# Optimization experiments

Measured on AMD Instinct MI355X. Metric: run time of the kernel, lower is better.

Reference implementation:

```python
import jax, jax.numpy as jnp
import numpy as np
import itertools

B = 262144  # batch of 16-d vectors to quantize

_BW = np.array([
    [4,0,0,0,0,0,0,0,0,0,0,0,0,0,0,0],[2,2,0,0,0,0,0,0,0,0,0,0,0,0,0,0],
    [2,0,2,0,0,0,0,0,0,0,0,0,0,0,0,0],[2,0,0,2,0,0,0,0,0,0,0,0,0,0,0,0],
    [2,0,0,0,2,0,0,0,0,0,0,0,0,0,0,0],[2,0,0,0,0,2,0,0,0,0,0,0,0,0,0,0],
    [2,0,0,0,0,0,2,0,0,0,0,0,0,0,0,0],[2,0,0,0,0,0,0,2,0,0,0,0,0,0,0,0],
    [2,0,0,0,0,0,0,0,2,0,0,0,0,0,0,0],[2,0,0,0,0,0,0,0,0,2,0,0,0,0,0,0],
    [2,0,0,0,0,0,0,0,0,0,2,0,0,0,0,0],[1,1,1,1,0,1,0,1,1,0,0,1,0,0,0,0],
    [0,1,1,1,1,0,1,0,1,1,0,0,1,0,0,0],[0,0,1,1,1,1,0,1,0,1,1,0,0,1,0,0],
    [0,0,0,1,1,1,1,0,1,0,1,1,0,0,1,0],[1,1,1,1,1,1,1,1,1,1,1,1,1,1,1,1]], dtype=np.float64)

_RM14_G = np.array([
    [1,1,1,1,0,1,0,1,1,0,0,1,0,0,0,0],
    [0,1,1,1,1,0,1,0,1,1,0,0,1,0,0,0],
    [0,0,1,1,1,1,0,1,0,1,1,0,0,1,0,0],
    [0,0,0,1,1,1,1,0,1,0,1,1,0,0,1,0],
    [1,1,1,1,1,1,1,1,1,1,1,1,1,1,1,1]], dtype=np.float64)


def _make_a_and_codebook():
    G = _BW
    vol = np.sqrt(np.linalg.det(G @ G.T))
    a = float(1.0 / vol ** (1.0 / 16.0))
    bits = np.array(list(itertools.product([0, 1], repeat=5)), dtype=np.float64)  # (32,5)
    C = bits @ _RM14_G  # (32,16)
    return a, C


def setup_inputs() -> dict:
    key = jax.random.key(0)
    a, C = _make_a_and_codebook()
    x_in = jax.random.normal(key, (B, 16), dtype=jnp.float32)
    return {
        "x_in": x_in,
        "C_rep": jnp.asarray(C, dtype=jnp.float32),
        "a": jnp.asarray([a], dtype=jnp.float32),
    }


def _d2_quantize(x_in):
    # Closest point in 2*D16: round x/2, fix parity by re-rounding the worst coord.
    x = x_in * 0.5                                   # (N,16)
    f = jnp.round(x)                                 # round-half-to-even, matches torch
    parity = jnp.mod(jnp.sum(f, axis=1), 2.0) == 1.0 # (N,)
    col = jnp.argmax(jnp.abs(x - f), axis=1)         # (N,) first max, matches torch
    onehot = col[:, None] == jnp.arange(x.shape[1])  # (N,16)
    xc = jnp.sum(jnp.where(onehot, x, 0.0), axis=1)  # x at worst coord
    fc = jnp.sum(jnp.where(onehot, f, 0.0), axis=1)  # f at worst coord
    corr = jnp.ceil(xc) + jnp.floor(xc) - fc         # flip rounding direction
    f = jnp.where(onehot & parity[:, None], corr[:, None], f)
    return 2.0 * f


def reference(x_in, C_rep, a):
    x = x_in / a                                     # (B,16)
    diffs = x[:, None, :] - C_rep[None, :, :]        # (B,32,16)
    fq = _d2_quantize(diffs.reshape(-1, 16)).reshape(-1, 32, 16)
    X = fq + C_rep[None, :, :]                       # (B,32,16) candidate points
    D = jnp.sum((X - x[:, None, :]) ** 2, axis=2)    # (B,32) squared distances
    idx = jnp.argmin(D, axis=1)                      # (B,)
    y = jnp.take_along_axis(X, idx[:, None, None], axis=1)[:, 0, :]
    return y * a
```

## Files before the change

kernel.cpp:

```cpp
#include <hip/hip_runtime.h>


constexpr int G5[5][16] = {
    {1,1,1,1,0,1,0,1,1,0,0,1,0,0,0,0},
    {0,1,1,1,1,0,1,0,1,1,0,0,1,0,0,0},
    {0,0,1,1,1,1,0,1,0,1,1,0,0,1,0,0},
    {0,0,0,1,1,1,1,0,1,0,1,1,0,0,1,0},
    {1,1,1,1,1,1,1,1,1,1,1,1,1,1,1,1}};

struct Tabs {
  int m[16];
  unsigned w[32];
  int pt[16];
};
constexpr Tabs make_tabs() {
  Tabs t{};
  for (int j = 0; j < 16; ++j) {
    int m = 0;
    for (int i = 0; i < 5; ++i) m |= G5[i][j] << (4 - i);
    t.m[j] = m;
    t.pt[j] = (G5[0][j] << 3) | (G5[1][j] << 2) | (G5[2][j] << 1) | G5[3][j];
  }
  for (int k = 0; k < 32; ++k) {
    unsigned om = 0, p2 = 0;
    for (int j = 0; j < 16; ++j) {
      int c = 0;
      for (int i = 0; i < 5; ++i) c += ((k >> (4 - i)) & 1) * G5[i][j];
      om |= (unsigned)(c & 1) << j;
      p2 ^= (unsigned)((c >> 1) & 1);
    }
    t.w[k] = om | (p2 << 16);
  }
  return t;
}
constexpr Tabs tb = make_tabs();

__device__ __forceinline__ int parity16i(const float (&f)[16]) {
  float s0 = ((f[0] + f[1]) + (f[2] + f[3])) + ((f[4] + f[5]) + (f[6] + f[7]));
  float s1 = ((f[8] + f[9]) + (f[10] + f[11])) + ((f[12] + f[13]) + (f[14] + f[15]));
  return ((int)(s0 + s1)) & 1;
}

template <bool EMIT>
__device__ __forceinline__ float eval_k(int kk, const float (&xh)[16], float a,
                                        float (&y)[16], const float (*Cs)[16]) {
#pragma clang fp contract(off)
  float cf[16];
  {
    const float4* crow = reinterpret_cast<const float4*>(&Cs[kk][0]);
    float4 c0 = crow[0], c1 = crow[1], c2 = crow[2], c3 = crow[3];
    cf[0] = c0.x; cf[1] = c0.y; cf[2] = c0.z; cf[3] = c0.w;
    cf[4] = c1.x; cf[5] = c1.y; cf[6] = c1.z; cf[7] = c1.w;
    cf[8] = c2.x; cf[9] = c2.y; cf[10] = c2.z; cf[11] = c2.w;
    cf[12] = c3.x; cf[13] = c3.y; cf[14] = c3.z; cf[15] = c3.w;
  }
  float f[16], dd[16];
#pragma unroll
  for (int j = 0; j < 16; ++j) {
    float x2 = __builtin_fmaf(cf[j], -0.5f, xh[j]);
    float fj = __builtin_rintf(x2);
    f[j] = fj;
    dd[j] = x2 - fj;
  }
  const int par = parity16i(f);

  float tv[16];
  int ti[16];
#pragma unroll
  for (int j = 0; j < 16; ++j) { tv[j] = __builtin_fabsf(dd[j]); ti[j] = 1 << j; }
#pragma unroll
  for (int w = 8; w >= 1; w >>= 1) {
#pragma unroll
    for (int j = 0; j < w; ++j) {
      bool L = tv[2 * j] >= tv[2 * j + 1];
      tv[j] = L ? tv[2 * j] : tv[2 * j + 1];
      ti[j] = L ? ti[2 * j] : ti[2 * j + 1];
    }
  }
  const int ohm = par ? ti[0] : 0;

  float sq[16];
#pragma unroll
  for (int j = 0; j < 16; ++j) {
    float X  = __builtin_fmaf(2.0f, f[j], cf[j]);
    float s2 = __builtin_copysignf(2.0f, dd[j]);
    float bitf = (float)((ohm >> j) & 1);
    float Xp = __builtin_fmaf(bitf, s2, X);
    float e  = __builtin_fmaf(-2.0f, xh[j], Xp);
    sq[j] = e * e;
    if (EMIT) y[j] = Xp * a;
  }
  float r0 = sq[0] + sq[8],  r1 = sq[1] + sq[9];
  float r2 = sq[2] + sq[10], r3 = sq[3] + sq[11];
  float r4 = sq[4] + sq[12], r5 = sq[5] + sq[13];
  float r6 = sq[6] + sq[14], r7 = sq[7] + sq[15];
  return ((r0 + r1) + (r2 + r3)) + ((r4 + r5) + (r6 + r7));
}

__global__ __launch_bounds__(256, 4) void bw_quant_kernel(
    const float* __restrict__ x_in,
    const float* __restrict__ C_rep,
    const float* __restrict__ a_ptr,
    float* __restrict__ y_out,
    int n_rows)
{
#pragma clang fp contract(off)
  __shared__ alignas(16) float Cs[32][16];
  for (int i = threadIdx.x; i < 32 * 16; i += 256)
    Cs[i >> 4][i & 15] = (float)__builtin_popcount((i >> 4) & tb.m[i & 15]);
  __syncthreads();

  const int row = blockIdx.x * 256 + threadIdx.x;
  if (row >= n_rows) return;

  const float a = a_ptr[0];

  float dd0[16], dd1[16], g[16], sq0[16];
  int P0 = 0, P1 = 0;
  {
    const float4* xr4 = reinterpret_cast<const float4*>(x_in + (size_t)row * 16);
    float xv[16];
#pragma unroll
    for (int q = 0; q < 4; ++q) {
      float4 v = xr4[q];
      xv[q * 4 + 0] = v.x; xv[q * 4 + 1] = v.y;
      xv[q * 4 + 2] = v.z; xv[q * 4 + 3] = v.w;
    }
#pragma unroll
    for (int j = 0; j < 16; ++j) {
      float xj = xv[j] / a;
      float xh = xj * 0.5f;
      float t0 = __builtin_rintf(xh);
      dd0[j] = xh - t0;
      float hm = xh - 0.5f;
      float t1 = __builtin_rintf(hm);
      dd1[j] = hm - t1;
      P0 |= ((int)t0 & 1) << j;
      P1 |= ((int)t1 & 1) << j;
      sq0[j] = dd0[j] * dd0[j];
      g[tb.pt[j]] = __builtin_fmaf(dd1[j], dd1[j], -sq0[j]);
    }
  }
  float S0 = (((sq0[0] + sq0[1]) + (sq0[2] + sq0[3])) + ((sq0[4] + sq0[5]) + (sq0[6] + sq0[7])))
           + (((sq0[8] + sq0[9]) + (sq0[10] + sq0[11])) + ((sq0[12] + sq0[13]) + (sq0[14] + sq0[15])));

#pragma unroll
  for (int s = 1; s < 16; s <<= 1) {
#pragma unroll
    for (int p = 0; p < 16; ++p) {
      if (!(p & s)) {
        float u = g[p], v = g[p | s];
        g[p] = u + v;
        g[p | s] = u - v;
      }
    }
  }
  float S1 = S0 + g[0];
  float h[16];
  h[0] = 0.0f;
#pragma unroll
  for (int t = 1; t < 16; ++t) h[t] = 0.5f * (g[0] - g[t]);

  float b1 = __builtin_inff(), b2 = b1, b3 = b1;
  int k1 = 0, k2 = 0, k3 = 0;

#pragma unroll
  for (int k = 0; k < 32; ++k) {
    const unsigned w = tb.w[k];
    const unsigned O = w & 0xFFFFu;
    const int p2 = (int)(w >> 16);
    const int kap = k >> 1;

    float s = (k & 1) ? (S1 - h[kap]) : (S0 + h[kap]);

    float d[16];
#pragma unroll
    for (int j = 0; j < 16; ++j)
      d[j] = ((O >> j) & 1u) ? dd1[j] : dd0[j];

    float t0 = __builtin_fmaxf(__builtin_fmaxf(__builtin_fabsf(d[0]),  __builtin_fabsf(d[1])),  __builtin_fabsf(d[2]));
    float t1 = __builtin_fmaxf(__builtin_fmaxf(__builtin_fabsf(d[3]),  __builtin_fabsf(d[4])),  __builtin_fabsf(d[5]));
    float t2 = __builtin_fmaxf(__builtin_fmaxf(__builtin_fabsf(d[6]),  __builtin_fabsf(d[7])),  __builtin_fabsf(d[8]));
    float t3 = __builtin_fmaxf(__builtin_fmaxf(__builtin_fabsf(d[9]),  __builtin_fabsf(d[10])), __builtin_fabsf(d[11]));
    float t4 = __builtin_fmaxf(__builtin_fmaxf(__builtin_fabsf(d[12]), __builtin_fabsf(d[13])), __builtin_fabsf(d[14]));
    float mx = __builtin_fmaxf(__builtin_fmaxf(__builtin_fmaxf(t0, t1), t2),
                               __builtin_fmaxf(__builtin_fmaxf(t3, t4), __builtin_fabsf(d[15])));

    unsigned sel = (O & (unsigned)P1) | (~O & (unsigned)P0);
    int cnt = __builtin_popcount(sel) + p2;
    float spen = s + __builtin_fmaf(-2.0f, mx, 1.0f);
    float dtil = (cnt & 1) ? spen : s;

    bool lt1 = dtil < b1, lt2 = dtil < b2, lt3 = dtil < b3;
    float nb3 = lt3 ? (lt2 ? b2 : dtil) : b3;  int nk3 = lt3 ? (lt2 ? k2 : k) : k3;
    float nb2 = lt2 ? (lt1 ? b1 : dtil) : b2;  int nk2 = lt2 ? (lt1 ? k1 : k) : k2;
    b3 = nb3; k3 = nk3;
    b2 = nb2; k2 = nk2;
    b1 = lt1 ? dtil : b1;  k1 = lt1 ? k : k1;
  }

  float xh[16];
  {
    const float4* xr4 = reinterpret_cast<const float4*>(x_in + (size_t)row * 16);
#pragma unroll
    for (int q = 0; q < 4; ++q) {
      float4 v = xr4[q];
      xh[q * 4 + 0] = (v.x / a) * 0.5f;
      xh[q * 4 + 1] = (v.y / a) * 0.5f;
      xh[q * 4 + 2] = (v.z / a) * 0.5f;
      xh[q * 4 + 3] = (v.w / a) * 0.5f;
    }
  }

  float ydummy[16];
  float D1 = eval_k<false>(k1, xh, a, ydummy, Cs);
  float D2 = eval_k<false>(k2, xh, a, ydummy, Cs);
  float D3 = eval_k<false>(k3, xh, a, ydummy, Cs);

  bool c2 = (D2 < D1) || (D2 == D1 && k2 < k1);
  float Db = c2 ? D2 : D1;
  int kb = c2 ? k2 : k1;
  bool c3 = (D3 < Db) || (D3 == Db && k3 < kb);
  kb = c3 ? k3 : kb;

  float y[16];
  (void)eval_k<true>(kb, xh, a, y, Cs);

  float4* yr4 = reinterpret_cast<float4*>(y_out + (size_t)row * 16);
#pragma unroll
  for (int q = 0; q < 4; ++q) {
    float4 v;
    v.x = y[q * 4 + 0]; v.y = y[q * 4 + 1];
    v.z = y[q * 4 + 2]; v.w = y[q * 4 + 3];
    yr4[q] = v;
  }
}

extern "C" void kernel_launch(void* const* d_in, const int* in_sizes, int n_in,
                              void* d_out, int out_size, void* d_ws, size_t ws_size,
                              hipStream_t stream) {
  const float* x_in  = (const float*)d_in[0];
  const float* C_rep = (const float*)d_in[1];
  const float* a_ptr = (const float*)d_in[2];
  float* y_out = (float*)d_out;

  const int n_rows = in_sizes[0] / 16;
  const int block = 256;
  const int grid = (n_rows + block - 1) / block;
  bw_quant_kernel<<<grid, block, 0, stream>>>(x_in, C_rep, a_ptr, y_out, n_rows);
}
```

Before: 24.33 us.

## Compute per-coset max and parity via butterfly transforms; drop the re-evaluation pass

Replaces the per-candidate 16-element select and max tree in the 32-coset loop with a Hadamard-style max butterfly over permuted |d0|/|d1| arrays, which yields the max for all 16 coset pairs at once. Parity per candidate is precomputed into a 32-bit mask from row-mask popcounts. The rescored top-3 candidates now emit their outputs directly instead of running a fourth evaluation. x/2 is staged in shared memory rather than reloaded and divided again. This adds 17 KB of LDS per block, which may limit occupancy, and keeps more live registers for the output candidates.

```diff
diff --git a/kernel.cpp b/kernel.cpp
--- a/kernel.cpp
+++ b/kernel.cpp
@@ -10,8 +10,9 @@
 
 struct Tabs {
   int m[16];
-  unsigned w[32];
   int pt[16];
+  unsigned rowm[5];
+  unsigned par2w;
 };
 constexpr Tabs make_tabs() {
   Tabs t{};
@@ -21,15 +22,20 @@
     t.m[j] = m;
     t.pt[j] = (G5[0][j] << 3) | (G5[1][j] << 2) | (G5[2][j] << 1) | G5[3][j];
   }
+  for (int i = 0; i < 5; ++i) {
+    unsigned rm = 0;
+    for (int j = 0; j < 16; ++j) rm |= (unsigned)G5[i][j] << j;
+    t.rowm[i] = rm;
+  }
+  t.par2w = 0;
   for (int k = 0; k < 32; ++k) {
-    unsigned om = 0, p2 = 0;
+    unsigned p2 = 0;
     for (int j = 0; j < 16; ++j) {
       int c = 0;
       for (int i = 0; i < 5; ++i) c += ((k >> (4 - i)) & 1) * G5[i][j];
-      om |= (unsigned)(c & 1) << j;
       p2 ^= (unsigned)((c >> 1) & 1);
     }
-    t.w[k] = om | (p2 << 16);
+    t.par2w |= p2 << k;
   }
   return t;
 }
@@ -41,7 +47,6 @@
   return ((int)(s0 + s1)) & 1;
 }
 
-template <bool EMIT>
 __device__ __forceinline__ float eval_k(int kk, const float (&xh)[16], float a,
                                         float (&y)[16], const float (*Cs)[16]) {
 #pragma clang fp contract(off)
@@ -88,7 +93,7 @@
     float Xp = __builtin_fmaf(bitf, s2, X);
     float e  = __builtin_fmaf(-2.0f, xh[j], Xp);
     sq[j] = e * e;
-    if (EMIT) y[j] = Xp * a;
+    y[j] = Xp * a;
   }
   float r0 = sq[0] + sq[8],  r1 = sq[1] + sq[9];
   float r2 = sq[2] + sq[10], r3 = sq[3] + sq[11];
@@ -106,6 +111,7 @@
 {
 #pragma clang fp contract(off)
   __shared__ alignas(16) float Cs[32][16];
+  __shared__ float XH[256][17];
   for (int i = threadIdx.x; i < 32 * 16; i += 256)
     Cs[i >> 4][i & 15] = (float)__builtin_popcount((i >> 4) & tb.m[i & 15]);
   __syncthreads();
@@ -114,8 +120,9 @@
   if (row >= n_rows) return;
 
   const float a = a_ptr[0];
-
-  float dd0[16], dd1[16], g[16], sq0[16];
+  const int tid = threadIdx.x;
+
+  float g[16], sq0[16], T[16], S[16];
   int P0 = 0, P1 = 0;
   {
     const float4* xr4 = reinterpret_cast<const float4*>(x_in + (size_t)row * 16);
@@ -130,28 +137,31 @@
     for (int j = 0; j < 16; ++j) {
       float xj = xv[j] / a;
       float xh = xj * 0.5f;
+      XH[tid][j] = xh;
       float t0 = __builtin_rintf(xh);
-      dd0[j] = xh - t0;
+      float d0 = xh - t0;
       float hm = xh - 0.5f;
       float t1 = __builtin_rintf(hm);
-      dd1[j] = hm - t1;
+      float d1 = hm - t1;
       P0 |= ((int)t0 & 1) << j;
       P1 |= ((int)t1 & 1) << j;
-      sq0[j] = dd0[j] * dd0[j];
-      g[tb.pt[j]] = __builtin_fmaf(dd1[j], dd1[j], -sq0[j]);
+      sq0[j] = d0 * d0;
+      g[tb.pt[j]] = __builtin_fmaf(d1, d1, -sq0[j]);
+      T[tb.pt[j]] = __builtin_fabsf(d0);
+      S[tb.pt[j]] = __builtin_fabsf(d1);
     }
   }
   float S0 = (((sq0[0] + sq0[1]) + (sq0[2] + sq0[3])) + ((sq0[4] + sq0[5]) + (sq0[6] + sq0[7])))
            + (((sq0[8] + sq0[9]) + (sq0[10] + sq0[11])) + ((sq0[12] + sq0[13]) + (sq0[14] + sq0[15])));
 
 #pragma unroll
-  for (int s = 1; s < 16; s <<= 1) {
+  for (int st = 1; st < 16; st <<= 1) {
 #pragma unroll
     for (int p = 0; p < 16; ++p) {
-      if (!(p & s)) {
-        float u = g[p], v = g[p | s];
+      if (!(p & st)) {
+        float u = g[p], v = g[p | st];
         g[p] = u + v;
-        g[p | s] = u - v;
+        g[p | st] = u - v;
       }
     }
   }
@@ -161,35 +171,42 @@
 #pragma unroll
   for (int t = 1; t < 16; ++t) h[t] = 0.5f * (g[0] - g[t]);
 
+#pragma unroll
+  for (int st = 1; st < 16; st <<= 1) {
+#pragma unroll
+    for (int p = 0; p < 16; ++p) {
+      if (!(p & st)) {
+        float tA = T[p], tB = T[p | st];
+        float sA = S[p], sB = S[p | st];
+        T[p]      = __builtin_fmaxf(tA, tB);
+        T[p | st] = __builtin_fmaxf(tA, sB);
+        S[p]      = __builtin_fmaxf(sA, sB);
+        S[p | st] = __builtin_fmaxf(sA, tB);
+      }
+    }
+  }
+
+  unsigned PAR;
+  {
+    unsigned Q = (unsigned)(P0 ^ P1);
+    PAR = ((__builtin_popcount((unsigned)P0) & 1) ? 0xFFFFFFFFu : 0u) ^ tb.par2w;
+    PAR ^= ((__builtin_popcount(Q & tb.rowm[0]) & 1) ? 0xFFFF0000u : 0u);
+    PAR ^= ((__builtin_popcount(Q & tb.rowm[1]) & 1) ? 0xFF00FF00u : 0u);
+    PAR ^= ((__builtin_popcount(Q & tb.rowm[2]) & 1) ? 0xF0F0F0F0u : 0u);
+    PAR ^= ((__builtin_popcount(Q & tb.rowm[3]) & 1) ? 0xCCCCCCCCu : 0u);
+    PAR ^= ((__builtin_popcount(Q & tb.rowm[4]) & 1) ? 0xAAAAAAAAu : 0u);
+  }
+
   float b1 = __builtin_inff(), b2 = b1, b3 = b1;
   int k1 = 0, k2 = 0, k3 = 0;
 
 #pragma unroll
   for (int k = 0; k < 32; ++k) {
-    const unsigned w = tb.w[k];
-    const unsigned O = w & 0xFFFFu;
-    const int p2 = (int)(w >> 16);
     const int kap = k >> 1;
-
-    float s = (k & 1) ? (S1 - h[kap]) : (S0 + h[kap]);
-
-    float d[16];
-#pragma unroll
-    for (int j = 0; j < 16; ++j)
-      d[j] = ((O >> j) & 1u) ? dd1[j] : dd0[j];
-
-    float t0 = __builtin_fmaxf(__builtin_fmaxf(__builtin_fabsf(d[0]),  __builtin_fabsf(d[1])),  __builtin_fabsf(d[2]));
-    float t1 = __builtin_fmaxf(__builtin_fmaxf(__builtin_fabsf(d[3]),  __builtin_fabsf(d[4])),  __builtin_fabsf(d[5]));
-    float t2 = __builtin_fmaxf(__builtin_fmaxf(__builtin_fabsf(d[6]),  __builtin_fabsf(d[7])),  __builtin_fabsf(d[8]));
-    float t3 = __builtin_fmaxf(__builtin_fmaxf(__builtin_fabsf(d[9]),  __builtin_fabsf(d[10])), __builtin_fabsf(d[11]));
-    float t4 = __builtin_fmaxf(__builtin_fmaxf(__builtin_fabsf(d[12]), __builtin_fabsf(d[13])), __builtin_fabsf(d[14]));
-    float mx = __builtin_fmaxf(__builtin_fmaxf(__builtin_fmaxf(t0, t1), t2),
-                               __builtin_fmaxf(__builtin_fmaxf(t3, t4), __builtin_fabsf(d[15])));
-
-    unsigned sel = (O & (unsigned)P1) | (~O & (unsigned)P0);
-    int cnt = __builtin_popcount(sel) + p2;
+    float s  = (k & 1) ? (S1 - h[kap]) : (S0 + h[kap]);
+    float mx = (k & 1) ? S[kap] : T[kap];
     float spen = s + __builtin_fmaf(-2.0f, mx, 1.0f);
-    float dtil = (cnt & 1) ? spen : s;
+    float dtil = ((PAR >> k) & 1u) ? spen : s;
 
     bool lt1 = dtil < b1, lt2 = dtil < b2, lt3 = dtil < b3;
     float nb3 = lt3 ? (lt2 ? b2 : dtil) : b3;  int nk3 = lt3 ? (lt2 ? k2 : k) : k3;
@@ -200,38 +217,32 @@
   }
 
   float xh[16];
-  {
-    const float4* xr4 = reinterpret_cast<const float4*>(x_in + (size_t)row * 16);
-#pragma unroll
-    for (int q = 0; q < 4; ++q) {
-      float4 v = xr4[q];
-      xh[q * 4 + 0] = (v.x / a) * 0.5f;
-      xh[q * 4 + 1] = (v.y / a) * 0.5f;
-      xh[q * 4 + 2] = (v.z / a) * 0.5f;
-      xh[q * 4 + 3] = (v.w / a) * 0.5f;
-    }
-  }
-
-  float ydummy[16];
-  float D1 = eval_k<false>(k1, xh, a, ydummy, Cs);
-  float D2 = eval_k<false>(k2, xh, a, ydummy, Cs);
-  float D3 = eval_k<false>(k3, xh, a, ydummy, Cs);
-
-  bool c2 = (D2 < D1) || (D2 == D1 && k2 < k1);
-  float Db = c2 ? D2 : D1;
-  int kb = c2 ? k2 : k1;
-  bool c3 = (D3 < Db) || (D3 == Db && k3 < kb);
-  kb = c3 ? k3 : kb;
-
-  float y[16];
-  (void)eval_k<true>(kb, xh, a, y, Cs);
+#pragma unroll
+  for (int j = 0; j < 16; ++j) xh[j] = XH[tid][j];
+
+  float yb[16], yt[16];
+  float Db = eval_k(k1, xh, a, yb, Cs);
+  int kb = k1;
+  {
+    float D2 = eval_k(k2, xh, a, yt, Cs);
+    bool c2 = (D2 < Db) || (D2 == Db && k2 < kb);
+    Db = c2 ? D2 : Db; kb = c2 ? k2 : kb;
+#pragma unroll
+    for (int j = 0; j < 16; ++j) yb[j] = c2 ? yt[j] : yb[j];
+  }
+  {
+    float D3 = eval_k(k3, xh, a, yt, Cs);
+    bool c3 = (D3 < Db) || (D3 == Db && k3 < kb);
+#pragma unroll
+    for (int j = 0; j < 16; ++j) yb[j] = c3 ? yt[j] : yb[j];
+  }
 
   float4* yr4 = reinterpret_cast<float4*>(y_out + (size_t)row * 16);
 #pragma unroll
   for (int q = 0; q < 4; ++q) {
     float4 v;
-    v.x = y[q * 4 + 0]; v.y = y[q * 4 + 1];
-    v.z = y[q * 4 + 2]; v.w = y[q * 4 + 3];
+    v.x = yb[q * 4 + 0]; v.y = yb[q * 4 + 1];
+    v.z = yb[q * 4 + 2]; v.w = yb[q * 4 + 3];
     yr4[q] = v;
   }
 }
```

Result: slower. 45.50 us (+87.0%).
